# Kernel optimization log

Measured on AMD Instinct MI355X. Metric: run time of the kernel, lower is better.

## Reference

```python
import jax, jax.numpy as jnp
import numpy as np

B, S, D = 2, 2048, 4096
NH, NKV, HD = 32, 8, 128
NREP = NH // NKV
ROPE_THETA = 10000.0


def setup_inputs() -> dict:
    key = jax.random.key(0)
    k1, k2, k3, k4, k5 = jax.random.split(key, 5)
    x = jax.random.normal(k1, (B, S, D), jnp.float32)
    wq = jax.random.normal(k2, (NH * HD, D), jnp.float32) * 0.02
    wk = jax.random.normal(k3, (NKV * HD, D), jnp.float32) * 0.02
    wv = jax.random.normal(k4, (NKV * HD, D), jnp.float32) * 0.02
    wo = jax.random.normal(k5, (D, NH * HD), jnp.float32) * 0.02
    inv_freq = 1.0 / (ROPE_THETA ** (np.arange(0, HD, 2, dtype=np.float64) / HD))
    ang = np.outer(np.arange(S, dtype=np.float64), inv_freq)  # [S, HD/2]
    return {
        'x': x, 'start_pos': 0,
        'freqs_cos': jnp.asarray(np.cos(ang), jnp.float32),
        'freqs_sin': jnp.asarray(np.sin(ang), jnp.float32),
        'wq': wq, 'wk': wk, 'wv': wv, 'wo': wo,
    }


def _apply_rope(x, cos, sin):
    # x: [B, S, H, HD]; cos/sin: [S, HD/2]. Matches torch view_as_complex on
    # interleaved (even, odd) feature pairs: (xr + i*xi) * (cos + i*sin).
    xr = x[..., 0::2]
    xi = x[..., 1::2]
    c = cos[None, :, None, :]
    s = sin[None, :, None, :]
    out_r = xr * c - xi * s
    out_i = xr * s + xi * c
    return jnp.stack([out_r, out_i], axis=-1).reshape(x.shape)


def reference(x, start_pos, freqs_cos, freqs_sin, wq, wk, wv, wo):
    b, s, _ = x.shape
    xq = (x @ wq.T).reshape(b, s, NH, HD)
    xk = (x @ wk.T).reshape(b, s, NKV, HD)
    xv = (x @ wv.T).reshape(b, s, NKV, HD)
    # Source applies RoPE to K and V (not Q) -- reproduced faithfully.
    xk = _apply_rope(xk, freqs_cos, freqs_sin)
    xv = _apply_rope(xv, freqs_cos, freqs_sin)
    # start_pos == 0 prefill: cache slice [:, :start_pos+s] == freshly written xk/xv.
    # repeat_kv: head h_out = h_kv * NREP + rep  ==  jnp.repeat along head axis.
    keys = jnp.repeat(xk, NREP, axis=2)    # [B, S, NH, HD]
    values = jnp.repeat(xv, NREP, axis=2)  # [B, S, NH, HD]
    scale = 1.0 / jnp.sqrt(jnp.asarray(HD, x.dtype))
    scores = jnp.einsum('bqhd,bkhd->bhqk', xq, keys) * scale  # [B, NH, S, S]
    probs = jax.nn.softmax(scores, axis=-1)  # NOTE: no causal mask in source
    out = jnp.einsum('bhqk,bkhd->bqhd', probs, values).reshape(b, s, NH * HD)
    return out @ wo.T
```

## Files before the change

kernel.cpp:

```cpp
#include <hip/hip_runtime.h>


typedef short bf16x8 __attribute__((ext_vector_type(8)));
typedef float f32x4 __attribute__((ext_vector_type(4)));

__device__ __forceinline__ void load16(const void* g, void* l) {
  __builtin_amdgcn_global_load_lds(
      (const __attribute__((address_space(1))) void*)g,
      (__attribute__((address_space(3))) void*)l, 16, 0, 0);
}

__device__ __forceinline__ f32x4 mfma16(bf16x8 a, bf16x8 b, f32x4 c) {
  return __builtin_amdgcn_mfma_f32_16x16x32_bf16(a, b, c, 0, 0, 0);
}

__device__ __forceinline__ unsigned short f2b(float f) {
  union { float f; unsigned int u; } v; v.f = f;
  unsigned int u = v.u;
  return (unsigned short)((u + 0x7fffu + ((u >> 16) & 1u)) >> 16);
}
__device__ __forceinline__ float b2f(unsigned short u) {
  union { unsigned int u; float f; } v; v.u = ((unsigned int)u) << 16;
  return v.f;
}

#define QSCALE (0.08838834764831845f * 1.4426950408889634f)

__global__ __launch_bounds__(256) void cvt_f32_bf16(
    const float* __restrict__ in, unsigned short* __restrict__ out, int n4) {
  int idx = blockIdx.x * 256 + threadIdx.x;
  int stride = gridDim.x * 256;
  for (int i = idx; i < n4; i += stride) {
    float4 v = reinterpret_cast<const float4*>(in)[i];
    ushort4 o;
    o.x = f2b(v.x); o.y = f2b(v.y); o.z = f2b(v.z); o.w = f2b(v.w);
    reinterpret_cast<ushort4*>(out)[i] = o;
  }
}

template <typename OutT, bool SCALEQ>
__global__ __launch_bounds__(512, 2) void gemm256(
    const unsigned short* __restrict__ A, const unsigned short* __restrict__ Bw,
    OutT* __restrict__ C, int M, int N, int K) {
  extern __shared__ char smem[];
  const int tid = threadIdx.x;
  const int lane = tid & 63;
  const int w = tid >> 6;
  const int lr = lane & 15, lg = lane >> 4;
  const int wr = w >> 2, wc = w & 3;

  const int nbn = N >> 8;
  const int bid = blockIdx.x, nwg = gridDim.x;
  const int swz = (bid & 7) * (nwg >> 3) + (bid >> 3);
  const int bm = swz / nbn, bn = swz % nbn;

  const unsigned short* Ab = A + (size_t)bm * 256 * K;
  const unsigned short* Bb = Bw + (size_t)bn * 256 * K;

  int mS[2], kS[2];
#pragma unroll
  for (int r = 0; r < 2; ++r) {
    int L = r * 8192 + tid * 16;
    int U = L ^ (((L >> 9) & 1) << 5);
    mS[r] = U >> 6;
    kS[r] = (U & 63) >> 1;
  }
  const int wavebase = (tid & ~63) * 16;

  f32x4 acc[8][4];
#pragma unroll
  for (int m = 0; m < 8; ++m)
#pragma unroll
    for (int n = 0; n < 4; ++n) acc[m][n] = (f32x4){0.f, 0.f, 0.f, 0.f};

#define STAGE_A(tt)                                                          \
  {                                                                          \
    char* dst = smem + ((tt)&3) * 32768;                                     \
    _Pragma("unroll") for (int r = 0; r < 2; ++r)                            \
        load16(Ab + (size_t)mS[r] * K + (tt)*32 + kS[r],                     \
               dst + r * 8192 + wavebase);                                   \
  }
#define STAGE_B(tt)                                                          \
  {                                                                          \
    char* dst = smem + ((tt)&3) * 32768 + 16384;                             \
    _Pragma("unroll") for (int r = 0; r < 2; ++r)                            \
        load16(Bb + (size_t)mS[r] * K + (tt)*32 + kS[r],                     \
               dst + r * 8192 + wavebase);                                   \
  }

  for (int tt = 0; tt < 3; ++tt) { STAGE_A(tt); STAGE_B(tt); }

  const int NT = K >> 5;
  const int xorb = ((lr >> 3) & 1) << 5;
  const int aRowBase = (wr * 128 + lr) * 64 + lg * 16;
  const int bRowBase = (wc * 64 + lr) * 64 + lg * 16;

  for (int t = 0; t < NT; ++t) {
    const int rem = NT - 1 - t;
    if (rem >= 2)      asm volatile("s_waitcnt vmcnt(8)" ::: "memory");
    else if (rem == 1) asm volatile("s_waitcnt vmcnt(4)" ::: "memory");
    else               asm volatile("s_waitcnt vmcnt(0)" ::: "memory");
    __builtin_amdgcn_s_barrier();

    const char* buf = smem + (t & 3) * 32768;
    bf16x8 a0[4], b0[4];
#pragma unroll
    for (int mf = 0; mf < 4; ++mf)
      a0[mf] = *(const bf16x8*)(buf + ((aRowBase + mf * 16 * 64) ^ xorb));
#pragma unroll
    for (int nf = 0; nf < 4; ++nf)
      b0[nf] = *(const bf16x8*)(buf + 16384 + ((bRowBase + nf * 16 * 64) ^ xorb));
    if (t + 3 < NT) STAGE_A(t + 3);
    __builtin_amdgcn_s_barrier();
    asm volatile("s_waitcnt lgkmcnt(0)" ::: "memory");
    __builtin_amdgcn_sched_barrier(0);
    __builtin_amdgcn_s_setprio(1);
#pragma unroll
    for (int mf = 0; mf < 4; ++mf)
#pragma unroll
      for (int nf = 0; nf < 4; ++nf)
        acc[mf][nf] = mfma16(a0[mf], b0[nf], acc[mf][nf]);
    __builtin_amdgcn_s_setprio(0);
    __builtin_amdgcn_s_barrier();
    bf16x8 a1[4];
#pragma unroll
    for (int mf = 0; mf < 4; ++mf)
      a1[mf] = *(const bf16x8*)(buf + ((aRowBase + (4 + mf) * 16 * 64) ^ xorb));
    if (t + 3 < NT) STAGE_B(t + 3);
    __builtin_amdgcn_s_barrier();
    asm volatile("s_waitcnt lgkmcnt(0)" ::: "memory");
    __builtin_amdgcn_sched_barrier(0);
    __builtin_amdgcn_s_setprio(1);
#pragma unroll
    for (int mf = 0; mf < 4; ++mf)
#pragma unroll
      for (int nf = 0; nf < 4; ++nf)
        acc[4 + mf][nf] = mfma16(a1[mf], b0[nf], acc[4 + mf][nf]);
    __builtin_amdgcn_s_setprio(0);
  }
#undef STAGE_A
#undef STAGE_B

#pragma unroll
  for (int mf = 0; mf < 8; ++mf)
#pragma unroll
    for (int nf = 0; nf < 4; ++nf)
#pragma unroll
      for (int r = 0; r < 4; ++r) {
        int rowc = bm * 256 + wr * 128 + mf * 16 + lg * 4 + r;
        int colc = bn * 256 + wc * 64 + nf * 16 + lr;
        float v = acc[mf][nf][r];
        if constexpr (SCALEQ) v *= QSCALE;
        if constexpr (sizeof(OutT) == 2)
          C[(size_t)rowc * N + colc] = (OutT)f2b(v);
        else
          C[(size_t)rowc * N + colc] = v;
      }
}

template <typename OutT>
__global__ __launch_bounds__(256) void gemm_bt(
    const unsigned short* __restrict__ A, const unsigned short* __restrict__ Bw,
    OutT* __restrict__ C, int M, int N, int K) {
  alignas(16) __shared__ unsigned short As[4][128][8];
  alignas(16) __shared__ unsigned short Bs[4][128][8];
  const int t = threadIdx.x;
  const int lane = t & 63, w = t >> 6;
  const int lr = lane & 15, lg = lane >> 4;
  const int wr = w >> 1, wc = w & 1;

  const int nbn = N >> 7;
  const int nwg = gridDim.x;
  const int bid = blockIdx.x;
  const int swz = (bid & 7) * (nwg >> 3) + (bid >> 3);
  const int bm = swz / nbn, bn = swz % nbn;

  f32x4 acc[4][4];
#pragma unroll
  for (int m = 0; m < 4; ++m)
#pragma unroll
    for (int n = 0; n < 4; ++n) acc[m][n] = (f32x4){0.f, 0.f, 0.f, 0.f};

  const int c0 = t, c1 = 256 + t;
  const int kc0 = c0 >> 7, row0 = c0 & 127;
  const int kc1 = c1 >> 7, row1 = c1 & 127;
  const unsigned short* Ab = A + (size_t)(bm * 128) * K;
  const unsigned short* Bb = Bw + (size_t)(bn * 128) * K;
  char* AsB = (char*)&As[0][0][0];
  char* BsB = (char*)&Bs[0][0][0];
  const int ub0 = (t & 192) * 16;
  const int ub1 = (256 + (t & 192)) * 16;

  for (int k0 = 0; k0 < K; k0 += 32) {
    load16(Ab + (size_t)row0 * K + k0 + kc0 * 8, AsB + ub0);
    load16(Ab + (size_t)row1 * K + k0 + kc1 * 8, AsB + ub1);
    load16(Bb + (size_t)row0 * K + k0 + kc0 * 8, BsB + ub0);
    load16(Bb + (size_t)row1 * K + k0 + kc1 * 8, BsB + ub1);
    __syncthreads();
    bf16x8 af[4], bfr[4];
#pragma unroll
    for (int i = 0; i < 4; ++i)
      af[i] = *(const bf16x8*)&As[lg][wr * 64 + i * 16 + lr][0];
#pragma unroll
    for (int i = 0; i < 4; ++i)
      bfr[i] = *(const bf16x8*)&Bs[lg][wc * 64 + i * 16 + lr][0];
#pragma unroll
    for (int m = 0; m < 4; ++m)
#pragma unroll
      for (int n = 0; n < 4; ++n)
        acc[m][n] = mfma16(af[m], bfr[n], acc[m][n]);
    __syncthreads();
  }

#pragma unroll
  for (int m = 0; m < 4; ++m)
#pragma unroll
    for (int n = 0; n < 4; ++n)
#pragma unroll
      for (int r = 0; r < 4; ++r) {
        int rowc = bm * 128 + wr * 64 + m * 16 + lg * 4 + r;
        int colc = bn * 128 + wc * 64 + n * 16 + lr;
        float v = acc[m][n][r];
        if constexpr (sizeof(OutT) == 2)
          C[(size_t)rowc * N + colc] = (OutT)f2b(v);
        else
          C[(size_t)rowc * N + colc] = v;
      }
}

__global__ __launch_bounds__(256) void rope_kv(
    const unsigned short* __restrict__ XKV,
    const float* __restrict__ fc, const float* __restrict__ fs,
    unsigned short* __restrict__ Kr, unsigned short* __restrict__ Vt) {
  __shared__ unsigned short Vl[128][66];
  const int t = threadIdx.x;
  const int bid = blockIdx.x;
  const int stile = bid & 31, bkv = bid >> 5;
  const int b = bkv >> 3, kvh = bkv & 7;
  const int s0 = stile * 64;
  const int l = t & 63;
  const int jrow = t >> 6;

  for (int j = 0; j < 16; ++j) {
    int s = s0 + j * 4 + jrow;
    ushort2 v = *(const ushort2*)(XKV + (size_t)(b * 2048 + s) * 2048 + kvh * 128 + 2 * l);
    float c = fc[s * 64 + l], sn = fs[s * 64 + l];
    float xr = b2f(v.x), xi = b2f(v.y);
    ushort2 o;
    o.x = f2b(xr * c - xi * sn);
    o.y = f2b(xr * sn + xi * c);
    *(ushort2*)(Kr + ((size_t)bkv * 2048 + s) * 128 + 2 * l) = o;
  }
  for (int j = 0; j < 16; ++j) {
    int ss = j * 4 + jrow;
    int s = s0 + ss;
    ushort2 v = *(const ushort2*)(XKV + (size_t)(b * 2048 + s) * 2048 + 1024 + kvh * 128 + 2 * l);
    float c = fc[s * 64 + l], sn = fs[s * 64 + l];
    float xr = b2f(v.x), xi = b2f(v.y);
    Vl[2 * l][ss] = f2b(xr * c - xi * sn);
    Vl[2 * l + 1][ss] = f2b(xr * sn + xi * c);
  }
  __syncthreads();
  const int d = t >> 1, half = t & 1;
  unsigned short* vdst = Vt + ((size_t)bkv * 128 + d) * 2048 + s0 + half * 32;
#pragma unroll
  for (int e = 0; e < 32; e += 4) {
    ushort4 pk;
    pk.x = Vl[d][half * 32 + e];
    pk.y = Vl[d][half * 32 + e + 1];
    pk.z = Vl[d][half * 32 + e + 2];
    pk.w = Vl[d][half * 32 + e + 3];
    *(ushort4*)(vdst + e) = pk;
  }
}

__global__ __launch_bounds__(256, 2) void attn_fwd(
    const unsigned short* __restrict__ XQ, const unsigned short* __restrict__ Kr,
    const unsigned short* __restrict__ Vt, unsigned short* __restrict__ AO) {
  extern __shared__ char smem[];
  char* Ksm = smem;
  char* Vsm = smem + 32768;
  unsigned short* Ps = (unsigned short*)(smem + 65536);
  const int t = threadIdx.x;
  const int lane = t & 63, w = t >> 6;
  const int lr = lane & 15, lg = lane >> 4;

  const int bid = blockIdx.x;
  const int nwg = gridDim.x;
  const int swz = (bid & 7) * (nwg >> 3) + (bid >> 3);
  const int qt = swz & 15;
  const int bh = swz >> 4;
  const int b = bh >> 5, h = bh & 31;
  const int bkv = b * 8 + (h >> 2);

  bf16x8 qf[2][4];
#pragma unroll
  for (int q2 = 0; q2 < 2; ++q2) {
    const unsigned short* qp =
        XQ + ((size_t)(b * 2048 + qt * 128 + w * 32 + q2 * 16 + lr)) * 4096 +
        h * 128 + lg * 8;
#pragma unroll
    for (int dc = 0; dc < 4; ++dc) qf[q2][dc] = *(const bf16x8*)(qp + dc * 32);
  }

  f32x4 acc[2][8];
#pragma unroll
  for (int q2 = 0; q2 < 2; ++q2)
#pragma unroll
    for (int i = 0; i < 8; ++i) acc[q2][i] = (f32x4){0.f, 0.f, 0.f, 0.f};
  float l_[2][4] = {{0.f, 0.f, 0.f, 0.f}, {0.f, 0.f, 0.f, 0.f}};

  const unsigned short* Kbase = Kr + (size_t)bkv * 2048 * 128;
  const unsigned short* Vbase = Vt + (size_t)bkv * 128 * 2048;

  int kK[4], dC[4], vD[4], vKc[4], dstb[4];
#pragma unroll
  for (int j = 0; j < 4; ++j) {
    const int c = t + j * 256;
    kK[j] = c & 63;  dC[j] = c >> 6;
    vD[j] = c & 127; vKc[j] = c >> 7;
    dstb[j] = (c & ~63) * 16;
  }

#define STAGE_KV(bufi, kt)                                                    \
  {                                                                           \
    char* kd = Ksm + (bufi)*16384;                                            \
    char* vd = Vsm + (bufi)*16384;                                            \
    _Pragma("unroll") for (int j = 0; j < 4; ++j) {                           \
      load16(Kbase + (size_t)((kt)*64 + kK[j]) * 128 + dC[j] * 8, kd + dstb[j]); \
      load16(Vbase + (size_t)vD[j] * 2048 + (kt)*64 + vKc[j] * 8, vd + dstb[j]); \
    }                                                                         \
  }

  STAGE_KV(0, 0);
  asm volatile("s_waitcnt vmcnt(0)" ::: "memory");
  __builtin_amdgcn_s_barrier();

  unsigned short* Pw = Ps + w * 2048;
  const int pbase = (lr >> 3) * 256 + (lr & 7);

  for (int kt = 0; kt < 32; ++kt) {
    const int cur = kt & 1;
    if (kt < 31) STAGE_KV(cur ^ 1, kt + 1);

    const char* Kc = Ksm + cur * 16384;
    const char* Vc = Vsm + cur * 16384;

#pragma unroll
    for (int nf = 0; nf < 4; ++nf) {
      f32x4 s0 = (f32x4){0.f, 0.f, 0.f, 0.f};
      f32x4 s1 = (f32x4){0.f, 0.f, 0.f, 0.f};
#pragma unroll
      for (int dc = 0; dc < 4; ++dc) {
        bf16x8 kf =
            *(const bf16x8*)(Kc + ((dc * 4 + lg) * 64 + nf * 16 + lr) * 16);
        s0 = mfma16(qf[0][dc], kf, s0);
        s1 = mfma16(qf[1][dc], kf, s1);
      }
      const int pb = pbase + nf * 512;
#pragma unroll
      for (int r = 0; r < 4; ++r) {
        float p0 = __builtin_amdgcn_exp2f(s0[r]);
        float p1 = __builtin_amdgcn_exp2f(s1[r]);
        l_[0][r] += p0;
        l_[1][r] += p1;
        Pw[pb + (lg * 4 + r) * 8] = f2b(p0);
        Pw[pb + (16 + lg * 4 + r) * 8] = f2b(p1);
      }
    }

#pragma unroll
    for (int ks = 0; ks < 2; ++ks) {
      bf16x8 pf0 = *(const bf16x8*)(Pw + (ks * 4 + lg) * 256 + lr * 8);
      bf16x8 pf1 = *(const bf16x8*)(Pw + (ks * 4 + lg) * 256 + (16 + lr) * 8);
#pragma unroll
      for (int dt = 0; dt < 8; ++dt) {
        bf16x8 vf =
            *(const bf16x8*)(Vc + ((ks * 4 + lg) * 128 + dt * 16 + lr) * 16);
        acc[0][dt] = mfma16(pf0, vf, acc[0][dt]);
        acc[1][dt] = mfma16(pf1, vf, acc[1][dt]);
      }
    }

    asm volatile("s_waitcnt vmcnt(0)" ::: "memory");
    __builtin_amdgcn_s_barrier();
  }
#undef STAGE_KV

#pragma unroll
  for (int q2 = 0; q2 < 2; ++q2)
#pragma unroll
    for (int r = 0; r < 4; ++r) {
#pragma unroll
      for (int o = 1; o < 16; o <<= 1) l_[q2][r] += __shfl_xor(l_[q2][r], o);
    }

#pragma unroll
  for (int q2 = 0; q2 < 2; ++q2)
#pragma unroll
    for (int r = 0; r < 4; ++r) {
      float inv = 1.f / l_[q2][r];
      size_t rowb =
          ((size_t)(b * 2048 + qt * 128 + w * 32 + q2 * 16 + lg * 4 + r)) * 4096 +
          h * 128;
#pragma unroll
      for (int dt = 0; dt < 8; ++dt)
        AO[rowb + dt * 16 + lr] = f2b(acc[q2][dt][r] * inv);
    }
}

extern "C" void kernel_launch(void* const* d_in, const int* in_sizes, int n_in,
                              void* d_out, int out_size, void* d_ws, size_t ws_size,
                              hipStream_t stream) {
  const float* x  = (const float*)d_in[0];
  const float* fc = (const float*)d_in[2];
  const float* fs = (const float*)d_in[3];
  const float* wq = (const float*)d_in[4];
  const float* wk = (const float*)d_in[5];
  const float* wv = (const float*)d_in[6];
  const float* wo = (const float*)d_in[7];

  const size_t MB = 1024ull * 1024ull;
  char* ws = (char*)d_ws;
  unsigned short* Xb  = (unsigned short*)(ws);
  unsigned short* Wsc = (unsigned short*)(ws + 32 * MB);
  unsigned short* XKV = (unsigned short*)(ws + 64 * MB);
  unsigned short* Kr  = (unsigned short*)(ws);
  unsigned short* Vt  = (unsigned short*)(ws + 8 * MB);
  unsigned short* AO  = (unsigned short*)(ws + 80 * MB);
  unsigned short* XQ  = (unsigned short*)d_out;

  (void)hipFuncSetAttribute((const void*)gemm256<unsigned short, true>,
                            hipFuncAttributeMaxDynamicSharedMemorySize, 131072);
  (void)hipFuncSetAttribute((const void*)gemm256<float, false>,
                            hipFuncAttributeMaxDynamicSharedMemorySize, 131072);
  (void)hipFuncSetAttribute((const void*)attn_fwd,
                            hipFuncAttributeMaxDynamicSharedMemorySize, 81920);

  dim3 blk(256);
  dim3 blk512(512);
  cvt_f32_bf16<<<2048, blk, 0, stream>>>(x, Xb, (2 * 2048 * 4096) / 4);
  cvt_f32_bf16<<<2048, blk, 0, stream>>>(wq, Wsc, (4096 * 4096) / 4);
  gemm256<unsigned short, true><<<256, blk512, 131072, stream>>>(
      Xb, Wsc, XQ, 4096, 4096, 4096);
  cvt_f32_bf16<<<2048, blk, 0, stream>>>(wk, Wsc, (1024 * 4096) / 4);
  cvt_f32_bf16<<<2048, blk, 0, stream>>>(wv, Wsc + 1024 * 4096, (1024 * 4096) / 4);
  gemm_bt<unsigned short><<<512, blk, 0, stream>>>(Xb, Wsc, XKV, 4096, 2048, 4096);
  rope_kv<<<512, blk, 0, stream>>>(XKV, fc, fs, Kr, Vt);
  attn_fwd<<<1024, blk, 81920, stream>>>(XQ, Kr, Vt, AO);
  cvt_f32_bf16<<<2048, blk, 0, stream>>>(wo, Wsc, (4096 * 4096) / 4);
  gemm256<float, false><<<256, blk512, 131072, stream>>>(
      AO, Wsc, (float*)d_out, 4096, 4096, 4096);
}
```

Baseline: 618.9 us.

## Restructure GEMM main loop to BK=64 double-buffered with quarter-phase MFMA schedule

The 256x256 bf16 GEMM moves from a K-tile of 32 with a 4-stage ring to a K-tile of 64 with two shared-memory buffers of 64 KB each. It also uses a new XOR swizzle over 8 16-byte chunks per 128-byte row. Each iteration now runs four MFMA phases over quarter tiles, interleaved with LDS fragment loads and next-tile global-to-LDS staging, with a full vmcnt(0) wait at the top. The intent is to halve loop iterations and barriers per unit of K and to reduce LDS bank conflicts. In exchange it gives up the deeper prefetch, so memory latency may be exposed, and the 128 KB of shared memory may limit occupancy to one block per CU.

```diff
diff --git a/kernel.cpp b/kernel.cpp
--- a/kernel.cpp
+++ b/kernel.cpp
@@ -54,18 +54,17 @@
   const int swz = (bid & 7) * (nwg >> 3) + (bid >> 3);
   const int bm = swz / nbn, bn = swz % nbn;
 
-  const unsigned short* Ab = A + (size_t)bm * 256 * K;
-  const unsigned short* Bb = Bw + (size_t)bn * 256 * K;
-
-  int mS[2], kS[2];
-#pragma unroll
-  for (int r = 0; r < 2; ++r) {
-    int L = r * 8192 + tid * 16;
-    int U = L ^ (((L >> 9) & 1) << 5);
-    mS[r] = U >> 6;
-    kS[r] = (U & 63) >> 1;
-  }
-  const int wavebase = (tid & ~63) * 16;
+  const unsigned short* Ag = A + (size_t)bm * 256 * K;
+  const unsigned short* Bg = Bw + (size_t)bn * 256 * K;
+
+  int srow[4], skhw[4], sdst[4];
+#pragma unroll
+  for (int j = 0; j < 4; ++j) {
+    const int c = tid + j * 512;
+    srow[j] = c >> 3;
+    skhw[j] = ((c & 7) ^ ((c >> 3) & 7)) << 3;
+    sdst[j] = ((tid & ~63) << 4) + j * 8192;
+  }
 
   f32x4 acc[8][4];
 #pragma unroll
@@ -73,44 +72,51 @@
 #pragma unroll
     for (int n = 0; n < 4; ++n) acc[m][n] = (f32x4){0.f, 0.f, 0.f, 0.f};
 
-#define STAGE_A(tt)                                                          \
-  {                                                                          \
-    char* dst = smem + ((tt)&3) * 32768;                                     \
-    _Pragma("unroll") for (int r = 0; r < 2; ++r)                            \
-        load16(Ab + (size_t)mS[r] * K + (tt)*32 + kS[r],                     \
-               dst + r * 8192 + wavebase);                                   \
-  }
-#define STAGE_B(tt)                                                          \
-  {                                                                          \
-    char* dst = smem + ((tt)&3) * 32768 + 16384;                             \
-    _Pragma("unroll") for (int r = 0; r < 2; ++r)                            \
-        load16(Bb + (size_t)mS[r] * K + (tt)*32 + kS[r],                     \
-               dst + r * 8192 + wavebase);                                   \
-  }
-
-  for (int tt = 0; tt < 3; ++tt) { STAGE_A(tt); STAGE_B(tt); }
-
-  const int NT = K >> 5;
-  const int xorb = ((lr >> 3) & 1) << 5;
-  const int aRowBase = (wr * 128 + lr) * 64 + lg * 16;
-  const int bRowBase = (wc * 64 + lr) * 64 + lg * 16;
+#define STAGEA4(tt)                                                           \
+  {                                                                           \
+    char* d = smem + (((tt)&1) * 65536);                                      \
+    _Pragma("unroll") for (int j = 0; j < 4; ++j)                             \
+        load16(Ag + (size_t)srow[j] * K + ((tt) << 6) + skhw[j], d + sdst[j]);\
+  }
+#define STAGEB4(tt)                                                           \
+  {                                                                           \
+    char* d = smem + (((tt)&1) * 65536) + 32768;                              \
+    _Pragma("unroll") for (int j = 0; j < 4; ++j)                             \
+        load16(Bg + (size_t)srow[j] * K + ((tt) << 6) + skhw[j], d + sdst[j]);\
+  }
+
+  STAGEB4(0);
+  STAGEA4(0);
+
+  const int NT = K >> 6;
+  const int rx = (lr & 7) << 4;
+  const int aRow0 = (wr * 128 + lr) * 128;
+  const int bRow0 = (wc * 64 + lr) * 128;
+  const int col0 = (lg * 16) ^ rx;
+  const int col1 = (64 + lg * 16) ^ rx;
+
+  bf16x8 aR[4][2], bR[4][2];
 
   for (int t = 0; t < NT; ++t) {
-    const int rem = NT - 1 - t;
-    if (rem >= 2)      asm volatile("s_waitcnt vmcnt(8)" ::: "memory");
-    else if (rem == 1) asm volatile("s_waitcnt vmcnt(4)" ::: "memory");
-    else               asm volatile("s_waitcnt vmcnt(0)" ::: "memory");
-    __builtin_amdgcn_s_barrier();
-
-    const char* buf = smem + (t & 3) * 32768;
-    bf16x8 a0[4], b0[4];
-#pragma unroll
-    for (int mf = 0; mf < 4; ++mf)
-      a0[mf] = *(const bf16x8*)(buf + ((aRowBase + mf * 16 * 64) ^ xorb));
-#pragma unroll
-    for (int nf = 0; nf < 4; ++nf)
-      b0[nf] = *(const bf16x8*)(buf + 16384 + ((bRowBase + nf * 16 * 64) ^ xorb));
-    if (t + 3 < NT) STAGE_A(t + 3);
+    const char* bufA = smem + (t & 1) * 65536;
+    const char* bufB = bufA + 32768;
+    const bool more = (t + 1) < NT;
+
+    asm volatile("s_waitcnt vmcnt(0)" ::: "memory");
+    __builtin_amdgcn_s_barrier();
+
+#pragma unroll
+    for (int mf = 0; mf < 4; ++mf) {
+      aR[mf][0] = *(const bf16x8*)(bufA + aRow0 + mf * 2048 + col0);
+      aR[mf][1] = *(const bf16x8*)(bufA + aRow0 + mf * 2048 + col1);
+    }
+#pragma unroll
+    for (int nf = 0; nf < 2; ++nf) {
+      bR[nf][0] = *(const bf16x8*)(bufB + bRow0 + nf * 2048 + col0);
+      bR[nf][1] = *(const bf16x8*)(bufB + bRow0 + nf * 2048 + col1);
+    }
+    if (more) STAGEB4(t + 1);
+    asm volatile("s_waitcnt lgkmcnt(8)" ::: "memory");
     __builtin_amdgcn_s_barrier();
     asm volatile("s_waitcnt lgkmcnt(0)" ::: "memory");
     __builtin_amdgcn_sched_barrier(0);
@@ -118,15 +124,19 @@
 #pragma unroll
     for (int mf = 0; mf < 4; ++mf)
 #pragma unroll
-      for (int nf = 0; nf < 4; ++nf)
-        acc[mf][nf] = mfma16(a0[mf], b0[nf], acc[mf][nf]);
+      for (int nf = 0; nf < 2; ++nf) {
+        acc[mf][nf] = mfma16(aR[mf][0], bR[nf][0], acc[mf][nf]);
+        acc[mf][nf] = mfma16(aR[mf][1], bR[nf][1], acc[mf][nf]);
+      }
     __builtin_amdgcn_s_setprio(0);
     __builtin_amdgcn_s_barrier();
-    bf16x8 a1[4];
-#pragma unroll
-    for (int mf = 0; mf < 4; ++mf)
-      a1[mf] = *(const bf16x8*)(buf + ((aRowBase + (4 + mf) * 16 * 64) ^ xorb));
-    if (t + 3 < NT) STAGE_B(t + 3);
+
+#pragma unroll
+    for (int nf = 2; nf < 4; ++nf) {
+      bR[nf][0] = *(const bf16x8*)(bufB + bRow0 + nf * 2048 + col0);
+      bR[nf][1] = *(const bf16x8*)(bufB + bRow0 + nf * 2048 + col1);
+    }
+    if (more) STAGEA4(t + 1);
     __builtin_amdgcn_s_barrier();
     asm volatile("s_waitcnt lgkmcnt(0)" ::: "memory");
     __builtin_amdgcn_sched_barrier(0);
@@ -134,12 +144,44 @@
 #pragma unroll
     for (int mf = 0; mf < 4; ++mf)
 #pragma unroll
-      for (int nf = 0; nf < 4; ++nf)
-        acc[4 + mf][nf] = mfma16(a1[mf], b0[nf], acc[4 + mf][nf]);
+      for (int nf = 2; nf < 4; ++nf) {
+        acc[mf][nf] = mfma16(aR[mf][0], bR[nf][0], acc[mf][nf]);
+        acc[mf][nf] = mfma16(aR[mf][1], bR[nf][1], acc[mf][nf]);
+      }
     __builtin_amdgcn_s_setprio(0);
-  }
-#undef STAGE_A
-#undef STAGE_B
+    __builtin_amdgcn_s_barrier();
+
+#pragma unroll
+    for (int mf = 0; mf < 4; ++mf) {
+      aR[mf][0] = *(const bf16x8*)(bufA + aRow0 + (4 + mf) * 2048 + col0);
+      aR[mf][1] = *(const bf16x8*)(bufA + aRow0 + (4 + mf) * 2048 + col1);
+    }
+    __builtin_amdgcn_s_barrier();
+    asm volatile("s_waitcnt lgkmcnt(0)" ::: "memory");
+    __builtin_amdgcn_sched_barrier(0);
+    __builtin_amdgcn_s_setprio(1);
+#pragma unroll
+    for (int mf = 0; mf < 4; ++mf)
+#pragma unroll
+      for (int nf = 0; nf < 2; ++nf) {
+        acc[4 + mf][nf] = mfma16(aR[mf][0], bR[nf][0], acc[4 + mf][nf]);
+        acc[4 + mf][nf] = mfma16(aR[mf][1], bR[nf][1], acc[4 + mf][nf]);
+      }
+    __builtin_amdgcn_s_setprio(0);
+    __builtin_amdgcn_s_barrier();
+
+    __builtin_amdgcn_s_setprio(1);
+#pragma unroll
+    for (int mf = 0; mf < 4; ++mf)
+#pragma unroll
+      for (int nf = 2; nf < 4; ++nf) {
+        acc[4 + mf][nf] = mfma16(aR[mf][0], bR[nf][0], acc[4 + mf][nf]);
+        acc[4 + mf][nf] = mfma16(aR[mf][1], bR[nf][1], acc[4 + mf][nf]);
+      }
+    __builtin_amdgcn_s_setprio(0);
+  }
+#undef STAGEA4
+#undef STAGEB4
 
 #pragma unroll
   for (int mf = 0; mf < 8; ++mf)
```

Result: faster. 597.6 us (-3.4%).
